# Optimization experiments

Measured on AMD Instinct MI355X. Metric: run time of the kernel, lower is better.

The kernel has to match this reference:

```python
import jax, jax.numpy as jnp
import numpy as np

B, T, D, H, L, F, V = 2, 512, 512, 8, 6, 2048, 32000
EPS = 1e-6


def _ln(x, g, b):
    m = x.mean(-1, keepdims=True)
    v = ((x - m) ** 2).mean(-1, keepdims=True)
    return (x - m) / jnp.sqrt(v + EPS) * g + b


def _mha(qx, kx, qkv_w, qkv_b, ow, ob, mask):
    # Wide heads: each head has dim D (Linear(D, H*D) projections, Linear(H*D, D) output).
    Bq, Tq, _ = qx.shape
    def proj(xx, w, bi):
        return (xx @ w + bi).reshape(Bq, Tq, H, D).transpose(0, 2, 1, 3)  # (B,H,T,D)
    q = proj(qx, qkv_w[0], qkv_b[0])
    k = proj(kx, qkv_w[1], qkv_b[1])
    v = proj(kx, qkv_w[2], qkv_b[2])
    s = jnp.einsum('bhqd,bhkd->bhqk', q, k) / jnp.sqrt(jnp.float32(D))
    if mask is not None:
        s = jnp.where(mask, s, -jnp.inf)
    w = jax.nn.softmax(s, axis=-1)
    o = jnp.einsum('bhqk,bhkd->bhqd', w, v).transpose(0, 2, 1, 3).reshape(Bq, Tq, H * D)
    return o @ ow + ob


def _pe(t, d):
    pos = jnp.arange(t, dtype=jnp.float32)[:, None]
    wl = jnp.exp(jnp.arange(0, d, 2, dtype=jnp.float32) / d * -jnp.log(10000.0))
    pe = jnp.zeros((t, d), dtype=jnp.float32)
    pe = pe.at[:, 0::2].set(jnp.sin(pos * wl))
    pe = pe.at[:, 1::2].set(jnp.cos(pos * wl))
    return pe


def _forward(x, y, enc_emb, dec_emb, enc_qkv_w, enc_qkv_b, enc_out_w, enc_out_b,
             enc_ln1_g, enc_ln1_b, enc_ff_w1, enc_ff_b1, enc_ff_w2, enc_ff_b2,
             enc_ln2_g, enc_ln2_b, dec_sa_qkv_w, dec_sa_qkv_b, dec_sa_out_w, dec_sa_out_b,
             dec_ln1_g, dec_ln1_b, dec_ca_qkv_w, dec_ca_qkv_b, dec_ca_out_w, dec_ca_out_b,
             dec_ln2_g, dec_ln2_b, dec_ff_w1, dec_ff_b1, dec_ff_w2, dec_ff_b2,
             dec_ln3_g, dec_ln3_b, head_w, head_b):
    pe = _pe(T, D)
    scale = jnp.sqrt(jnp.float32(D))
    # ---- encoder ----
    h = enc_emb[x] * scale + pe  # (B,T,D)
    for i in range(L):
        a = _mha(h, h, enc_qkv_w[i], enc_qkv_b[i], enc_out_w[i], enc_out_b[i], None)
        h = _ln(a + h, enc_ln1_g[i], enc_ln1_b[i])
        f = jax.nn.relu(h @ enc_ff_w1[i] + enc_ff_b1[i]) @ enc_ff_w2[i] + enc_ff_b2[i]
        h = _ln(f + h, enc_ln2_g[i], enc_ln2_b[i])
    # ---- decoder ----
    causal = jnp.tril(jnp.ones((T, T), dtype=bool))[None, None]  # (1,1,T,T)
    d = dec_emb[y] * scale + pe
    for i in range(L):
        a = _mha(d, d, dec_sa_qkv_w[i], dec_sa_qkv_b[i], dec_sa_out_w[i], dec_sa_out_b[i], causal)
        d = _ln(a + d, dec_ln1_g[i], dec_ln1_b[i])
        c = _mha(d, h, dec_ca_qkv_w[i], dec_ca_qkv_b[i], dec_ca_out_w[i], dec_ca_out_b[i], None)
        d = _ln(c + d, dec_ln2_g[i], dec_ln2_b[i])
        f = jax.nn.relu(d @ dec_ff_w1[i] + dec_ff_b1[i]) @ dec_ff_w2[i] + dec_ff_b2[i]
        d = _ln(f + d, dec_ln3_g[i], dec_ln3_b[i])
    return d @ head_w + head_b  # (B,T,V) logits


def setup_inputs() -> dict:
    key = jax.random.key(0)
    ks = iter(jax.random.split(key, 40))
    def nrm(shape):
        return jax.random.normal(next(ks), shape, dtype=jnp.float32) * 0.02
    HD = H * D
    return {
        'x': jax.random.randint(next(ks), (B, T), 0, V, dtype=jnp.int32),
        'y': jax.random.randint(next(ks), (B, T), 0, V, dtype=jnp.int32),
        'enc_emb': nrm((V, D)), 'dec_emb': nrm((V, D)),
        'enc_qkv_w': nrm((L, 3, D, HD)), 'enc_qkv_b': jnp.zeros((L, 3, HD)),
        'enc_out_w': nrm((L, HD, D)), 'enc_out_b': jnp.zeros((L, D)),
        'enc_ln1_g': jnp.ones((L, D)), 'enc_ln1_b': jnp.zeros((L, D)),
        'enc_ff_w1': nrm((L, D, F)), 'enc_ff_b1': jnp.zeros((L, F)),
        'enc_ff_w2': nrm((L, F, D)), 'enc_ff_b2': jnp.zeros((L, D)),
        'enc_ln2_g': jnp.ones((L, D)), 'enc_ln2_b': jnp.zeros((L, D)),
        'dec_sa_qkv_w': nrm((L, 3, D, HD)), 'dec_sa_qkv_b': jnp.zeros((L, 3, HD)),
        'dec_sa_out_w': nrm((L, HD, D)), 'dec_sa_out_b': jnp.zeros((L, D)),
        'dec_ln1_g': jnp.ones((L, D)), 'dec_ln1_b': jnp.zeros((L, D)),
        'dec_ca_qkv_w': nrm((L, 3, D, HD)), 'dec_ca_qkv_b': jnp.zeros((L, 3, HD)),
        'dec_ca_out_w': nrm((L, HD, D)), 'dec_ca_out_b': jnp.zeros((L, D)),
        'dec_ln2_g': jnp.ones((L, D)), 'dec_ln2_b': jnp.zeros((L, D)),
        'dec_ff_w1': nrm((L, D, F)), 'dec_ff_b1': jnp.zeros((L, F)),
        'dec_ff_w2': nrm((L, F, D)), 'dec_ff_b2': jnp.zeros((L, D)),
        'dec_ln3_g': jnp.ones((L, D)), 'dec_ln3_b': jnp.zeros((L, D)),
        'head_w': nrm((D, V)), 'head_b': jnp.zeros((V,)),
    }


def reference(x, y, enc_emb, dec_emb, enc_qkv_w, enc_qkv_b, enc_out_w, enc_out_b,
              enc_ln1_g, enc_ln1_b, enc_ff_w1, enc_ff_b1, enc_ff_w2, enc_ff_b2,
              enc_ln2_g, enc_ln2_b, dec_sa_qkv_w, dec_sa_qkv_b, dec_sa_out_w, dec_sa_out_b,
              dec_ln1_g, dec_ln1_b, dec_ca_qkv_w, dec_ca_qkv_b, dec_ca_out_w, dec_ca_out_b,
              dec_ln2_g, dec_ln2_b, dec_ff_w1, dec_ff_b1, dec_ff_w2, dec_ff_b2,
              dec_ln3_g, dec_ln3_b, head_w, head_b):
    return _forward(x, y, enc_emb, dec_emb, enc_qkv_w, enc_qkv_b, enc_out_w, enc_out_b,
                    enc_ln1_g, enc_ln1_b, enc_ff_w1, enc_ff_b1, enc_ff_w2, enc_ff_b2,
                    enc_ln2_g, enc_ln2_b, dec_sa_qkv_w, dec_sa_qkv_b, dec_sa_out_w, dec_sa_out_b,
                    dec_ln1_g, dec_ln1_b, dec_ca_qkv_w, dec_ca_qkv_b, dec_ca_out_w, dec_ca_out_b,
                    dec_ln2_g, dec_ln2_b, dec_ff_w1, dec_ff_b1, dec_ff_w2, dec_ff_b2,
                    dec_ln3_g, dec_ln3_b, head_w, head_b)
```

## Files before the change

kernel.cpp:

```cpp
#include <hip/hip_runtime.h>
#include <hip/hip_bf16.h>

#define B_ 2
#define T_ 512
#define D_ 512
#define H_ 8
#define L_ 6
#define F_ 2048
#define V_ 32000
#define BT_ (B_ * T_)
#define HD_ (H_ * D_)
#define BH_ (B_ * H_)

typedef __attribute__((ext_vector_type(8))) short short8;
typedef __attribute__((ext_vector_type(4))) short short4v;
typedef __attribute__((ext_vector_type(4))) float f32x4;

__device__ __forceinline__ short f2b(float f) {
  __hip_bfloat16 h = __float2bfloat16(f);
  short u; __builtin_memcpy(&u, &h, 2); return u;
}
__device__ __forceinline__ void store_c(float* p, float v) { *p = v; }
__device__ __forceinline__ void store_c(short* p, float v) { *p = f2b(v); }

__global__ __launch_bounds__(256) void embed_kernel(
    const int* __restrict__ tok, const float* __restrict__ emb,
    float* __restrict__ out, short* __restrict__ out16)
{
  const int row = blockIdx.x;
  const int t = row & (T_ - 1);
  const int token = tok[row];
  const float* e = emb + (size_t)token * D_;
  float* o = out + (size_t)row * D_;
  short* o16 = out16 + (size_t)row * D_;
  const float scale = sqrtf((float)D_);
  const float nl = -logf(10000.0f);
  for (int d = threadIdx.x; d < D_; d += 256) {
    int i = d >> 1;
    float wl = expf(nl * (2.0f * (float)i) / (float)D_);
    float ang = (float)t * wl;
    float pe = (d & 1) ? cosf(ang) : sinf(ang);
    float v = e[d] * scale + pe;
    o[d] = v; o16[d] = f2b(v);
  }
}

template<bool BTM, typename OutT, int BM>
__global__ __launch_bounds__(256, 3) void mfma_gemm(
    const short* __restrict__ A, long lda, long a_hi, long a_lo,
    const void* __restrict__ Bv, long ldb, long b_hi, long b_lo,
    OutT* __restrict__ C, long ldc, long c_hi, long c_lo, long pstride,
    short* __restrict__ Ct, int trans_hh,
    int K, int nh, int ksplit, float scale,
    const float* __restrict__ bias, long bias_stride)
{
  constexpr int SA = BM + 1;
  constexpr int AU = BM / 32;
  constexpr int WRN = (BM == 128) ? 2 : 1;
  constexpr int WN  = 128 / (4 / WRN);
  constexpr int NR  = WN / 16;
  __shared__ short8 As8[8 * SA];
  __shared__ short8 Bs8[8 * 129];
  const int tid = threadIdx.x;
  const int bh = blockIdx.z / ksplit;
  const int kz = blockIdx.z - bh * ksplit;
  const int bb = bh / nh, hh = bh - bb * nh;
  const short* Ab = A + (long)bb * a_hi + (long)hh * a_lo;
  const short* Bbs = (const short*)Bv + (long)bb * b_hi + (long)hh * b_lo;
  const float* Bbf = (const float*)Bv + (long)bb * b_hi + (long)hh * b_lo;
  OutT* Cb = C + (long)bb * c_hi + (long)hh * c_lo + (long)kz * pstride;

  const int gx = gridDim.x, gy = gridDim.y;
  const int nwg = gx * gy;
  int lin = blockIdx.y * gx + blockIdx.x;
  {
    const int xcd = lin & 7, idx = lin >> 3;
    const int q = nwg >> 3, r = nwg & 7;
    lin = (xcd < r ? xcd * (q + 1) : r * (q + 1) + (xcd - r) * q) + idx;
  }
  const int bn = (lin / gy) * 128;
  const int bm = (lin % gy) * BM;

  const int klen = K / ksplit, kbase = kz * klen;
  const int lane = tid & 63, wid = tid >> 6;
  const int wr = (WRN == 2) ? (wid >> 1) : 0;
  const int wc = (WRN == 2) ? (wid & 1) : wid;
  const int lg = lane >> 4, r16 = lane & 15;

  int arow[AU], acol[AU];
#pragma unroll
  for (int u = 0; u < AU; ++u) { int o = u * 256 + tid; arow[u] = o >> 3; acol[u] = o & 7; }
  const int ncol = tid & 127, nsh = tid >> 7;

  short8 pa[AU];
  short8 pbt[4];
  float  pbn[4][8];

  auto load = [&](int k0) {
#pragma unroll
    for (int u = 0; u < AU; ++u)
      pa[u] = *(const short8*)(Ab + (long)(bm + arow[u]) * lda + (k0 + acol[u] * 8));
    if constexpr (BTM) {
#pragma unroll
      for (int u = 0; u < 4; ++u)
        pbt[u] = *(const short8*)(Bbs + (long)(bn + (u * 256 + tid) / 8) * ldb + (k0 + ((u * 256 + tid) & 7) * 8));
    } else {
      const float* s = Bbf + (long)(k0 + nsh * 32) * ldb + (bn + ncol);
#pragma unroll
      for (int i = 0; i < 4; ++i)
#pragma unroll
        for (int j = 0; j < 8; ++j)
          pbn[i][j] = s[(long)(i * 8 + j) * ldb];
    }
  };
  auto stage = [&]() {
#pragma unroll
    for (int u = 0; u < AU; ++u) As8[acol[u] * SA + arow[u]] = pa[u];
    if constexpr (BTM) {
#pragma unroll
      for (int u = 0; u < 4; ++u)
        Bs8[((u * 256 + tid) & 7) * 129 + (u * 256 + tid) / 8] = pbt[u];
    } else {
#pragma unroll
      for (int i = 0; i < 4; ++i) {
        short8 v;
#pragma unroll
        for (int j = 0; j < 8; ++j) v[j] = f2b(pbn[i][j]);
        Bs8[(nsh * 4 + i) * 129 + ncol] = v;
      }
    }
  };

  f32x4 acc[4][NR] = {};
  auto domfma = [&]() {
#pragma unroll
    for (int kb = 0; kb < 2; ++kb) {
      const int cha = (kb * 4 + lg) * SA;
      const int chb = (kb * 4 + lg) * 129;
      short8 a0 = As8[cha + wr * 64 +  0 + r16];
      short8 a1 = As8[cha + wr * 64 + 16 + r16];
      short8 a2 = As8[cha + wr * 64 + 32 + r16];
      short8 a3 = As8[cha + wr * 64 + 48 + r16];
#pragma unroll
      for (int n = 0; n < NR; ++n) {
        short8 bfr = Bs8[chb + wc * WN + n * 16 + r16];
        acc[0][n] = __builtin_amdgcn_mfma_f32_16x16x32_bf16(a0, bfr, acc[0][n], 0, 0, 0);
        acc[1][n] = __builtin_amdgcn_mfma_f32_16x16x32_bf16(a1, bfr, acc[1][n], 0, 0, 0);
        acc[2][n] = __builtin_amdgcn_mfma_f32_16x16x32_bf16(a2, bfr, acc[2][n], 0, 0, 0);
        acc[3][n] = __builtin_amdgcn_mfma_f32_16x16x32_bf16(a3, bfr, acc[3][n], 0, 0, 0);
      }
    }
  };

  load(kbase);
  stage();
  __syncthreads();
  const int nsteps = klen >> 6;
  for (int t = 0; t < nsteps; ++t) {
    const bool more = (t + 1 < nsteps);
    if (more) load(kbase + (t + 1) * 64);
    domfma();
    if (more) { __syncthreads(); stage(); __syncthreads(); }
  }

  const float* bp = bias ? bias + (long)hh * bias_stride : nullptr;
  if (hh == trans_hh) {
#pragma unroll
    for (int m = 0; m < 4; ++m)
#pragma unroll
      for (int n = 0; n < NR; ++n) {
        const int col = bn + wc * WN + n * 16 + r16;
        const float badd = bp ? bp[col] : 0.0f;
        short4v sv;
#pragma unroll
        for (int rr = 0; rr < 4; ++rr) sv[rr] = f2b(acc[m][n][rr] * scale + badd);
        *(short4v*)(Ct + (long)col * BT_ + (bm + wr * 64 + m * 16 + lg * 4)) = sv;
      }
  } else {
#pragma unroll
    for (int m = 0; m < 4; ++m)
#pragma unroll
      for (int rr = 0; rr < 4; ++rr) {
        const int row = bm + wr * 64 + m * 16 + lg * 4 + rr;
        OutT* crow = Cb + (long)row * ldc + bn + wc * WN + r16;
#pragma unroll
        for (int n = 0; n < NR; ++n) {
          float v = acc[m][n][rr] * scale;
          if (bp) v += bp[bn + wc * WN + n * 16 + r16];
          store_c(&crow[n * 16], v);
        }
      }
  }
}

__global__ __launch_bounds__(256) void reduce_bias_relu_bf16(
    const float* __restrict__ P, long pstride, int ks,
    const float* __restrict__ bias, short* __restrict__ out, long mn, int N)
{
  const long i = ((long)blockIdx.x * 256 + threadIdx.x) * 4;
  if (i >= mn) return;
  float4 s = *(const float4*)(P + i);
  for (int z = 1; z < ks; ++z) {
    float4 t = *(const float4*)(P + (long)z * pstride + i);
    s.x += t.x; s.y += t.y; s.z += t.z; s.w += t.w;
  }
  const int col = (int)(i % N);
  s.x += bias[col]; s.y += bias[col + 1]; s.z += bias[col + 2]; s.w += bias[col + 3];
  short4v o;
  o[0] = f2b(fmaxf(s.x, 0.f)); o[1] = f2b(fmaxf(s.y, 0.f));
  o[2] = f2b(fmaxf(s.z, 0.f)); o[3] = f2b(fmaxf(s.w, 0.f));
  *(short4v*)(out + i) = o;
}

__global__ __launch_bounds__(256) void reduce_ln_kernel(
    const float* __restrict__ P, long pstride, int ks,
    const float* __restrict__ bias, float* __restrict__ hbuf, short* __restrict__ h16,
    const float* __restrict__ gam, const float* __restrict__ bet)
{
  __shared__ float red[256];
  const int row = blockIdx.x, tid = threadIdx.x;
  const long base = (long)row * D_;
  float s0 = hbuf[base + tid] + bias[tid];
  float s1 = hbuf[base + tid + 256] + bias[tid + 256];
  for (int z = 0; z < ks; ++z) {
    s0 += P[(long)z * pstride + base + tid];
    s1 += P[(long)z * pstride + base + tid + 256];
  }
  red[tid] = s0 + s1; __syncthreads();
  for (int o = 128; o > 0; o >>= 1) { if (tid < o) red[tid] += red[tid + o]; __syncthreads(); }
  const float mean = red[0] * (1.0f / D_); __syncthreads();
  const float d0 = s0 - mean, d1 = s1 - mean;
  red[tid] = d0 * d0 + d1 * d1; __syncthreads();
  for (int o = 128; o > 0; o >>= 1) { if (tid < o) red[tid] += red[tid + o]; __syncthreads(); }
  const float inv = rsqrtf(red[0] * (1.0f / D_) + 1e-6f);
  const float v0 = d0 * inv * gam[tid] + bet[tid];
  const float v1 = d1 * inv * gam[tid + 256] + bet[tid + 256];
  hbuf[base + tid] = v0;       h16[base + tid] = f2b(v0);
  hbuf[base + tid + 256] = v1; h16[base + tid + 256] = f2b(v1);
}

__global__ __launch_bounds__(256) void softmax_kernel(
    const float* __restrict__ S, short* __restrict__ P, int causal)
{
  __shared__ float red[256];
  const int q = blockIdx.x, bh = blockIdx.y, tid = threadIdx.x;
  const float* row = S + ((size_t)bh * T_ + q) * T_;
  short* prow = P + ((size_t)bh * T_ + q) * T_;
  const int n = causal ? (q + 1) : T_;
  const float v0 = row[tid], v1 = row[tid + 256];
  const bool in0 = tid < n, in1 = (tid + 256) < n;
  red[tid] = fmaxf(in0 ? v0 : -3.0e38f, in1 ? v1 : -3.0e38f);
  __syncthreads();
  for (int o = 128; o > 0; o >>= 1) { if (tid < o) red[tid] = fmaxf(red[tid], red[tid + o]); __syncthreads(); }
  const float m = red[0]; __syncthreads();
  const float e0 = in0 ? expf(v0 - m) : 0.0f;
  const float e1 = in1 ? expf(v1 - m) : 0.0f;
  red[tid] = e0 + e1; __syncthreads();
  for (int o = 128; o > 0; o >>= 1) { if (tid < o) red[tid] += red[tid + o]; __syncthreads(); }
  const float inv = 1.0f / red[0];
  prow[tid] = f2b(e0 * inv);
  prow[tid + 256] = f2b(e1 * inv);
}

extern "C" void kernel_launch(void* const* d_in, const int* in_sizes, int n_in,
                              void* d_out, int out_size, void* d_ws, size_t ws_size,
                              hipStream_t stream)
{
  const int*   x         = (const int*)d_in[0];
  const int*   y         = (const int*)d_in[1];
  const float* enc_emb   = (const float*)d_in[2];
  const float* dec_emb   = (const float*)d_in[3];
  const float* enc_qkv_w = (const float*)d_in[4];
  const float* enc_qkv_b = (const float*)d_in[5];
  const float* enc_out_w = (const float*)d_in[6];
  const float* enc_out_b = (const float*)d_in[7];
  const float* enc_ln1_g = (const float*)d_in[8];
  const float* enc_ln1_b = (const float*)d_in[9];
  const float* enc_ff_w1 = (const float*)d_in[10];
  const float* enc_ff_b1 = (const float*)d_in[11];
  const float* enc_ff_w2 = (const float*)d_in[12];
  const float* enc_ff_b2 = (const float*)d_in[13];
  const float* enc_ln2_g = (const float*)d_in[14];
  const float* enc_ln2_b = (const float*)d_in[15];
  const float* dec_sa_qkv_w = (const float*)d_in[16];
  const float* dec_sa_qkv_b = (const float*)d_in[17];
  const float* dec_sa_out_w = (const float*)d_in[18];
  const float* dec_sa_out_b = (const float*)d_in[19];
  const float* dec_ln1_g = (const float*)d_in[20];
  const float* dec_ln1_b = (const float*)d_in[21];
  const float* dec_ca_qkv_w = (const float*)d_in[22];
  const float* dec_ca_qkv_b = (const float*)d_in[23];
  const float* dec_ca_out_w = (const float*)d_in[24];
  const float* dec_ca_out_b = (const float*)d_in[25];
  const float* dec_ln2_g = (const float*)d_in[26];
  const float* dec_ln2_b = (const float*)d_in[27];
  const float* dec_ff_w1 = (const float*)d_in[28];
  const float* dec_ff_b1 = (const float*)d_in[29];
  const float* dec_ff_w2 = (const float*)d_in[30];
  const float* dec_ff_b2 = (const float*)d_in[31];
  const float* dec_ln3_g = (const float*)d_in[32];
  const float* dec_ln3_b = (const float*)d_in[33];
  const float* head_w    = (const float*)d_in[34];
  const float* head_b    = (const float*)d_in[35];
  float* out = (float*)d_out;

  char* wsb = (char*)d_ws;
  size_t off = 0;
  auto carve = [&](size_t bytes) { char* p = wsb + off; off += (bytes + 255) & ~255ull; return p; };
  float* h    = (float*)carve((size_t)BT_ * D_ * 4);
  float* dd   = (float*)carve((size_t)BT_ * D_ * 4);
  short* hb16 = (short*)carve((size_t)BT_ * D_ * 2);
  short* db16 = (short*)carve((size_t)BT_ * D_ * 2);
  short* Qb   = (short*)carve((size_t)BT_ * HD_ * 2);
  short* Kb   = (short*)carve((size_t)BT_ * HD_ * 2);
  short* Vt   = (short*)carve((size_t)HD_ * BT_ * 2);
  float* Sb   = (float*)carve((size_t)BH_ * T_ * T_ * 4);
  short* Pb   = (short*)carve((size_t)BH_ * T_ * T_ * 2);
  short* Ob   = Qb;
  short* mid  = Qb;
  (void)ws_size;

  dim3 blk(256);
  const long TT  = (long)T_ * T_;
  const long THD = (long)T_ * HD_;
  const long WQKV = (long)D_ * HD_;

  auto gemm = [&](bool bt, bool of32, bool bm64,
                  const short* A, long lda, long a_hi, long a_lo,
                  const void* Bp, long ldb, long b_hi, long b_lo,
                  void* Cp, long ldc, long c_hi, long c_lo, long pstride,
                  short* Ct, int trans_hh,
                  int M, int N, int K, int batch, int nh, int ksplit,
                  float scale, const float* bias, long bstride) {
    dim3 grd(N / 128, M / (bm64 ? 64 : 128), batch * ksplit);
    if (bm64) {
      if (bt) {
        if (of32) mfma_gemm<true , float, 64><<<grd, blk, 0, stream>>>(A, lda, a_hi, a_lo, Bp, ldb, b_hi, b_lo,
            (float*)Cp, ldc, c_hi, c_lo, pstride, Ct, trans_hh, K, nh, ksplit, scale, bias, bstride);
        else      mfma_gemm<true , short, 64><<<grd, blk, 0, stream>>>(A, lda, a_hi, a_lo, Bp, ldb, b_hi, b_lo,
            (short*)Cp, ldc, c_hi, c_lo, pstride, Ct, trans_hh, K, nh, ksplit, scale, bias, bstride);
      } else {
        if (of32) mfma_gemm<false, float, 64><<<grd, blk, 0, stream>>>(A, lda, a_hi, a_lo, Bp, ldb, b_hi, b_lo,
            (float*)Cp, ldc, c_hi, c_lo, pstride, Ct, trans_hh, K, nh, ksplit, scale, bias, bstride);
        else      mfma_gemm<false, short, 64><<<grd, blk, 0, stream>>>(A, lda, a_hi, a_lo, Bp, ldb, b_hi, b_lo,
            (short*)Cp, ldc, c_hi, c_lo, pstride, Ct, trans_hh, K, nh, ksplit, scale, bias, bstride);
      }
    } else {
      if (of32) mfma_gemm<false, float, 128><<<grd, blk, 0, stream>>>(A, lda, a_hi, a_lo, Bp, ldb, b_hi, b_lo,
          (float*)Cp, ldc, c_hi, c_lo, pstride, Ct, trans_hh, K, nh, ksplit, scale, bias, bstride);
      else      mfma_gemm<false, short, 128><<<grd, blk, 0, stream>>>(A, lda, a_hi, a_lo, Bp, ldb, b_hi, b_lo,
          (short*)Cp, ldc, c_hi, c_lo, pstride, Ct, trans_hh, K, nh, ksplit, scale, bias, bstride);
    }
  };

  auto attention = [&](const short* qsrc, const short* kvsrc, bool self,
                       const float* qkvw, const float* qkvb,
                       const float* ow, const float* ob,
                       float* resid, short* resid16, int causal,
                       const float* lng, const float* lnb) {
    if (self) {
      gemm(false, false, true, qsrc, D_, 0, 0, qkvw, HD_, 0, WQKV,
           Qb, HD_, 0, (long)(Kb - Qb), 0, Vt, 2,
           BT_, HD_, D_, 3, 3, 1, 1.0f, qkvb, HD_);
    } else {
      gemm(false, false, true, qsrc, D_, 0, 0, qkvw, HD_, 0, 0,
           Qb, HD_, 0, 0, 0, nullptr, -1,
           BT_, HD_, D_, 1, 1, 1, 1.0f, qkvb, 0);
      gemm(false, false, true, kvsrc, D_, 0, 0, qkvw + WQKV, HD_, 0, WQKV,
           Kb, HD_, 0, 0, 0, Vt, 1,
           BT_, HD_, D_, 2, 2, 1, 1.0f, qkvb + HD_, HD_);
    }
    gemm(true, true, true, Qb, HD_, THD, D_, Kb, HD_, THD, D_,
         Sb, T_, (long)H_ * TT, TT, 0, nullptr, -1,
         T_, T_, D_, BH_, H_, 1, 0.044194173824159216f, nullptr, 0);
    softmax_kernel<<<dim3(T_, BH_), blk, 0, stream>>>(Sb, Pb, causal);
    gemm(true, false, true, Pb, T_, (long)H_ * TT, TT, Vt, BT_, T_, (long)D_ * BT_,
         Ob, HD_, THD, D_, 0, nullptr, -1,
         T_, D_, T_, BH_, H_, 1, 1.0f, nullptr, 0);
    gemm(false, true, true, Ob, HD_, 0, 0, ow, D_, 0, 0,
         Sb, D_, 0, 0, (long)BT_ * D_, nullptr, -1,
         BT_, D_, HD_, 1, 1, 8, 1.0f, nullptr, 0);
    reduce_ln_kernel<<<dim3(BT_), blk, 0, stream>>>(
        Sb, (long)BT_ * D_, 8, ob, resid, resid16, lng, lnb);
  };

  auto ffn = [&](float* resid, short* resid16,
                 const float* w1, const float* b1,
                 const float* w2, const float* b2,
                 const float* lng, const float* lnb) {
    gemm(false, true, true, resid16, D_, 0, 0, w1, F_, 0, 0,
         Sb, F_, 0, 0, (long)BT_ * F_, nullptr, -1,
         BT_, F_, D_, 1, 1, 2, 1.0f, nullptr, 0);
    reduce_bias_relu_bf16<<<dim3(BT_ * F_ / 1024), blk, 0, stream>>>(
        Sb, (long)BT_ * F_, 2, b1, mid, (long)BT_ * F_, F_);
    gemm(false, true, true, mid, F_, 0, 0, w2, D_, 0, 0,
         Sb, D_, 0, 0, (long)BT_ * D_, nullptr, -1,
         BT_, D_, F_, 1, 1, 8, 1.0f, nullptr, 0);
    reduce_ln_kernel<<<dim3(BT_), blk, 0, stream>>>(
        Sb, (long)BT_ * D_, 8, b2, resid, resid16, lng, lnb);
  };

  embed_kernel<<<dim3(BT_), blk, 0, stream>>>(x, enc_emb, h, hb16);
  for (int i = 0; i < L_; ++i) {
    attention(hb16, hb16, true,
              enc_qkv_w + (size_t)i * 3 * WQKV, enc_qkv_b + (size_t)i * 3 * HD_,
              enc_out_w + (size_t)i * HD_ * D_, enc_out_b + (size_t)i * D_,
              h, hb16, 0, enc_ln1_g + (size_t)i * D_, enc_ln1_b + (size_t)i * D_);
    ffn(h, hb16, enc_ff_w1 + (size_t)i * D_ * F_, enc_ff_b1 + (size_t)i * F_,
        enc_ff_w2 + (size_t)i * F_ * D_, enc_ff_b2 + (size_t)i * D_,
        enc_ln2_g + (size_t)i * D_, enc_ln2_b + (size_t)i * D_);
  }

  embed_kernel<<<dim3(BT_), blk, 0, stream>>>(y, dec_emb, dd, db16);
  for (int i = 0; i < L_; ++i) {
    attention(db16, db16, true,
              dec_sa_qkv_w + (size_t)i * 3 * WQKV, dec_sa_qkv_b + (size_t)i * 3 * HD_,
              dec_sa_out_w + (size_t)i * HD_ * D_, dec_sa_out_b + (size_t)i * D_,
              dd, db16, 1, dec_ln1_g + (size_t)i * D_, dec_ln1_b + (size_t)i * D_);
    attention(db16, hb16, false,
              dec_ca_qkv_w + (size_t)i * 3 * WQKV, dec_ca_qkv_b + (size_t)i * 3 * HD_,
              dec_ca_out_w + (size_t)i * HD_ * D_, dec_ca_out_b + (size_t)i * D_,
              dd, db16, 0, dec_ln2_g + (size_t)i * D_, dec_ln2_b + (size_t)i * D_);
    ffn(dd, db16, dec_ff_w1 + (size_t)i * D_ * F_, dec_ff_b1 + (size_t)i * F_,
        dec_ff_w2 + (size_t)i * F_ * D_, dec_ff_b2 + (size_t)i * D_,
        dec_ln3_g + (size_t)i * D_, dec_ln3_b + (size_t)i * D_);
  }

  gemm(false, true, false, db16, D_, 0, 0, head_w, V_, 0, 0,
       out, V_, 0, 0, 0, nullptr, -1,
       BT_, V_, D_, 1, 1, 1, 1.0f, head_b, 0);
}
```

Baseline: 2.392 ms.

## Fuse softmax into PV GEMM, skip causal tiles, fuse FFN bias+ReLU, reduce split-K

```diff
diff --git a/kernel.cpp b/kernel.cpp
--- a/kernel.cpp
+++ b/kernel.cpp
@@ -50,14 +50,14 @@
     const short* __restrict__ A, long lda, long a_hi, long a_lo,
     const void* __restrict__ Bv, long ldb, long b_hi, long b_lo,
     OutT* __restrict__ C, long ldc, long c_hi, long c_lo, long pstride,
-    short* __restrict__ Ct, int trans_hh,
+    short* __restrict__ Ct, int trans_hh, int relu, int causal_skip,
     int K, int nh, int ksplit, float scale,
     const float* __restrict__ bias, long bias_stride)
 {
   constexpr int SA = BM + 1;
   constexpr int AU = BM / 32;
   constexpr int WRN = (BM == 128) ? 2 : 1;
-  constexpr int WN  = 128 / (4 / WRN);
+  constexpr int WN  = (BM == 128) ? 64 : 32;
   constexpr int NR  = WN / 16;
   __shared__ short8 As8[8 * SA];
   __shared__ short8 Bs8[8 * 129];
@@ -80,6 +80,7 @@
   }
   const int bn = (lin / gy) * 128;
   const int bm = (lin % gy) * BM;
+  if (causal_skip && bn > bm + BM - 1) return;
 
   const int klen = K / ksplit, kbase = kz * klen;
   const int lane = tid & 63, wid = tid >> 6;
@@ -90,6 +91,9 @@
   int arow[AU], acol[AU];
 #pragma unroll
   for (int u = 0; u < AU; ++u) { int o = u * 256 + tid; arow[u] = o >> 3; acol[u] = o & 7; }
+  int brow[4], bcol[4];
+#pragma unroll
+  for (int u = 0; u < 4; ++u) { int o = u * 256 + tid; brow[u] = o >> 3; bcol[u] = o & 7; }
   const int ncol = tid & 127, nsh = tid >> 7;
 
   short8 pa[AU];
@@ -103,7 +107,7 @@
     if constexpr (BTM) {
 #pragma unroll
       for (int u = 0; u < 4; ++u)
-        pbt[u] = *(const short8*)(Bbs + (long)(bn + (u * 256 + tid) / 8) * ldb + (k0 + ((u * 256 + tid) & 7) * 8));
+        pbt[u] = *(const short8*)(Bbs + (long)(bn + brow[u]) * ldb + (k0 + bcol[u] * 8));
     } else {
       const float* s = Bbf + (long)(k0 + nsh * 32) * ldb + (bn + ncol);
 #pragma unroll
@@ -118,8 +122,7 @@
     for (int u = 0; u < AU; ++u) As8[acol[u] * SA + arow[u]] = pa[u];
     if constexpr (BTM) {
 #pragma unroll
-      for (int u = 0; u < 4; ++u)
-        Bs8[((u * 256 + tid) & 7) * 129 + (u * 256 + tid) / 8] = pbt[u];
+      for (int u = 0; u < 4; ++u) Bs8[bcol[u] * 129 + brow[u]] = pbt[u];
     } else {
 #pragma unroll
       for (int i = 0; i < 4; ++i) {
@@ -187,29 +190,155 @@
         for (int n = 0; n < NR; ++n) {
           float v = acc[m][n][rr] * scale;
           if (bp) v += bp[bn + wc * WN + n * 16 + r16];
+          if (relu) v = fmaxf(v, 0.0f);
           store_c(&crow[n * 16], v);
         }
       }
   }
 }
 
-__global__ __launch_bounds__(256) void reduce_bias_relu_bf16(
-    const float* __restrict__ P, long pstride, int ks,
-    const float* __restrict__ bias, short* __restrict__ out, long mn, int N)
+__global__ __launch_bounds__(256, 3) void smpv_kernel(
+    const float* __restrict__ S, const short* __restrict__ Vt,
+    short* __restrict__ O, int causal)
 {
-  const long i = ((long)blockIdx.x * 256 + threadIdx.x) * 4;
-  if (i >= mn) return;
-  float4 s = *(const float4*)(P + i);
-  for (int z = 1; z < ks; ++z) {
-    float4 t = *(const float4*)(P + (long)z * pstride + i);
-    s.x += t.x; s.y += t.y; s.z += t.z; s.w += t.w;
-  }
-  const int col = (int)(i % N);
-  s.x += bias[col]; s.y += bias[col + 1]; s.z += bias[col + 2]; s.w += bias[col + 3];
-  short4v o;
-  o[0] = f2b(fmaxf(s.x, 0.f)); o[1] = f2b(fmaxf(s.y, 0.f));
-  o[2] = f2b(fmaxf(s.z, 0.f)); o[3] = f2b(fmaxf(s.w, 0.f));
-  *(short4v*)(out + i) = o;
+  __shared__ short8 As8[8 * 65];
+  __shared__ short8 Bs8[8 * 129];
+  __shared__ float mrow[64], linv[64];
+
+  const int tid = threadIdx.x;
+  const int bh = blockIdx.z;
+  const int b = bh >> 3, hh = bh & 7;
+  const int bm = blockIdx.y * 64;
+  const int bn = blockIdx.x * 128;
+  const int lane = tid & 63, w4 = tid >> 6;
+  const int lg = lane >> 4, r16 = lane & 15;
+
+  const float* Sb = S + (long)bh * T_ * T_;
+  const short* Vb = Vt + ((long)hh * D_ + bn) * BT_ + (long)b * T_;
+
+  {
+    const int row = tid >> 2, sub = tid & 3;
+    const int qrow = bm + row;
+    const int ncols = causal ? (qrow + 1) : T_;
+    const float* sp = Sb + (long)qrow * T_;
+    float mx = -3.0e38f;
+    for (int i = 0; i < 32; ++i) {
+      const int c0 = (sub + i * 4) * 4;
+      if (c0 < ncols) {
+        float4 v = *(const float4*)(sp + c0);
+        mx = fmaxf(mx, v.x);
+        if (c0 + 1 < ncols) mx = fmaxf(mx, v.y);
+        if (c0 + 2 < ncols) mx = fmaxf(mx, v.z);
+        if (c0 + 3 < ncols) mx = fmaxf(mx, v.w);
+      }
+    }
+    mx = fmaxf(mx, __shfl_xor(mx, 1));
+    mx = fmaxf(mx, __shfl_xor(mx, 2));
+    float sm = 0.0f;
+    for (int i = 0; i < 32; ++i) {
+      const int c0 = (sub + i * 4) * 4;
+      if (c0 < ncols) {
+        float4 v = *(const float4*)(sp + c0);
+        sm += expf(v.x - mx);
+        if (c0 + 1 < ncols) sm += expf(v.y - mx);
+        if (c0 + 2 < ncols) sm += expf(v.z - mx);
+        if (c0 + 3 < ncols) sm += expf(v.w - mx);
+      }
+    }
+    sm += __shfl_xor(sm, 1);
+    sm += __shfl_xor(sm, 2);
+    if (sub == 0) { mrow[row] = mx; linv[row] = 1.0f / sm; }
+  }
+  __syncthreads();
+
+  int arow[2], acol[2];
+#pragma unroll
+  for (int u = 0; u < 2; ++u) { int o = u * 256 + tid; arow[u] = o >> 3; acol[u] = o & 7; }
+  int brow[4], bcol[4];
+#pragma unroll
+  for (int u = 0; u < 4; ++u) { int o = u * 256 + tid; brow[u] = o >> 3; bcol[u] = o & 7; }
+
+  float4 pa[2][2];
+  short8 pbt[4];
+
+  auto load = [&](int k0) {
+#pragma unroll
+    for (int u = 0; u < 2; ++u) {
+      const float* s = Sb + (long)(bm + arow[u]) * T_ + (k0 + acol[u] * 8);
+      pa[u][0] = *(const float4*)(s);
+      pa[u][1] = *(const float4*)(s + 4);
+    }
+#pragma unroll
+    for (int u = 0; u < 4; ++u)
+      pbt[u] = *(const short8*)(Vb + (long)brow[u] * BT_ + (k0 + bcol[u] * 8));
+  };
+  auto stage = [&](int k0, bool mask) {
+#pragma unroll
+    for (int u = 0; u < 2; ++u) {
+      const int row = arow[u];
+      const int qrow = bm + row;
+      const float m = mrow[row];
+      const float vals[8] = {pa[u][0].x, pa[u][0].y, pa[u][0].z, pa[u][0].w,
+                             pa[u][1].x, pa[u][1].y, pa[u][1].z, pa[u][1].w};
+      short8 v;
+#pragma unroll
+      for (int j = 0; j < 8; ++j) {
+        const bool valid = !mask || (k0 + acol[u] * 8 + j <= qrow);
+        v[j] = f2b(valid ? expf(vals[j] - m) : 0.0f);
+      }
+      As8[acol[u] * 65 + row] = v;
+    }
+#pragma unroll
+    for (int u = 0; u < 4; ++u) Bs8[bcol[u] * 129 + brow[u]] = pbt[u];
+  };
+
+  f32x4 acc[4][2] = {};
+  auto domfma = [&]() {
+#pragma unroll
+    for (int kb = 0; kb < 2; ++kb) {
+      const int cha = (kb * 4 + lg) * 65;
+      const int chb = (kb * 4 + lg) * 129;
+      short8 a0 = As8[cha +  0 + r16];
+      short8 a1 = As8[cha + 16 + r16];
+      short8 a2 = As8[cha + 32 + r16];
+      short8 a3 = As8[cha + 48 + r16];
+#pragma unroll
+      for (int n = 0; n < 2; ++n) {
+        short8 bfr = Bs8[chb + w4 * 32 + n * 16 + r16];
+        acc[0][n] = __builtin_amdgcn_mfma_f32_16x16x32_bf16(a0, bfr, acc[0][n], 0, 0, 0);
+        acc[1][n] = __builtin_amdgcn_mfma_f32_16x16x32_bf16(a1, bfr, acc[1][n], 0, 0, 0);
+        acc[2][n] = __builtin_amdgcn_mfma_f32_16x16x32_bf16(a2, bfr, acc[2][n], 0, 0, 0);
+        acc[3][n] = __builtin_amdgcn_mfma_f32_16x16x32_bf16(a3, bfr, acc[3][n], 0, 0, 0);
+      }
+    }
+  };
+
+  const int nsteps = causal ? ((bm >> 6) + 1) : (T_ >> 6);
+  load(0);
+  stage(0, causal && (0 >= bm));
+  __syncthreads();
+  for (int t = 0; t < nsteps; ++t) {
+    const bool more = (t + 1 < nsteps);
+    if (more) load((t + 1) * 64);
+    domfma();
+    if (more) {
+      __syncthreads();
+      stage((t + 1) * 64, causal && ((t + 1) * 64 >= bm));
+      __syncthreads();
+    }
+  }
+
+  short* Ob = O + ((long)b * T_ + bm) * HD_ + hh * D_ + bn;
+#pragma unroll
+  for (int m = 0; m < 4; ++m)
+#pragma unroll
+    for (int rr = 0; rr < 4; ++rr) {
+      const int row = m * 16 + lg * 4 + rr;
+      const float il = linv[row];
+#pragma unroll
+      for (int n = 0; n < 2; ++n)
+        Ob[(long)row * HD_ + w4 * 32 + n * 16 + r16] = f2b(acc[m][n][rr] * il);
+    }
 }
 
 __global__ __launch_bounds__(256) void reduce_ln_kernel(
@@ -237,29 +366,6 @@
   const float v1 = d1 * inv * gam[tid + 256] + bet[tid + 256];
   hbuf[base + tid] = v0;       h16[base + tid] = f2b(v0);
   hbuf[base + tid + 256] = v1; h16[base + tid + 256] = f2b(v1);
-}
-
-__global__ __launch_bounds__(256) void softmax_kernel(
-    const float* __restrict__ S, short* __restrict__ P, int causal)
-{
-  __shared__ float red[256];
-  const int q = blockIdx.x, bh = blockIdx.y, tid = threadIdx.x;
-  const float* row = S + ((size_t)bh * T_ + q) * T_;
-  short* prow = P + ((size_t)bh * T_ + q) * T_;
-  const int n = causal ? (q + 1) : T_;
-  const float v0 = row[tid], v1 = row[tid + 256];
-  const bool in0 = tid < n, in1 = (tid + 256) < n;
-  red[tid] = fmaxf(in0 ? v0 : -3.0e38f, in1 ? v1 : -3.0e38f);
-  __syncthreads();
-  for (int o = 128; o > 0; o >>= 1) { if (tid < o) red[tid] = fmaxf(red[tid], red[tid + o]); __syncthreads(); }
-  const float m = red[0]; __syncthreads();
-  const float e0 = in0 ? expf(v0 - m) : 0.0f;
-  const float e1 = in1 ? expf(v1 - m) : 0.0f;
-  red[tid] = e0 + e1; __syncthreads();
-  for (int o = 128; o > 0; o >>= 1) { if (tid < o) red[tid] += red[tid + o]; __syncthreads(); }
-  const float inv = 1.0f / red[0];
-  prow[tid] = f2b(e0 * inv);
-  prow[tid + 256] = f2b(e1 * inv);
 }
 
 extern "C" void kernel_launch(void* const* d_in, const int* in_sizes, int n_in,
@@ -315,7 +421,6 @@
   short* Kb   = (short*)carve((size_t)BT_ * HD_ * 2);
   short* Vt   = (short*)carve((size_t)HD_ * BT_ * 2);
   float* Sb   = (float*)carve((size_t)BH_ * T_ * T_ * 4);
-  short* Pb   = (short*)carve((size_t)BH_ * T_ * T_ * 2);
   short* Ob   = Qb;
   short* mid  = Qb;
   (void)ws_size;
@@ -325,7 +430,7 @@
   const long THD = (long)T_ * HD_;
   const long WQKV = (long)D_ * HD_;
 
-  auto gemm = [&](bool bt, bool of32, bool bm64,
+  auto gemm = [&](bool bt, bool of32, bool bm64, int relu, int cskip,
                   const short* A, long lda, long a_hi, long a_lo,
                   const void* Bp, long ldb, long b_hi, long b_lo,
                   void* Cp, long ldc, long c_hi, long c_lo, long pstride,
@@ -336,20 +441,20 @@
     if (bm64) {
       if (bt) {
         if (of32) mfma_gemm<true , float, 64><<<grd, blk, 0, stream>>>(A, lda, a_hi, a_lo, Bp, ldb, b_hi, b_lo,
-            (float*)Cp, ldc, c_hi, c_lo, pstride, Ct, trans_hh, K, nh, ksplit, scale, bias, bstride);
+            (float*)Cp, ldc, c_hi, c_lo, pstride, Ct, trans_hh, relu, cskip, K, nh, ksplit, scale, bias, bstride);
         else      mfma_gemm<true , short, 64><<<grd, blk, 0, stream>>>(A, lda, a_hi, a_lo, Bp, ldb, b_hi, b_lo,
-            (short*)Cp, ldc, c_hi, c_lo, pstride, Ct, trans_hh, K, nh, ksplit, scale, bias, bstride);
+            (short*)Cp, ldc, c_hi, c_lo, pstride, Ct, trans_hh, relu, cskip, K, nh, ksplit, scale, bias, bstride);
       } else {
         if (of32) mfma_gemm<false, float, 64><<<grd, blk, 0, stream>>>(A, lda, a_hi, a_lo, Bp, ldb, b_hi, b_lo,
-            (float*)Cp, ldc, c_hi, c_lo, pstride, Ct, trans_hh, K, nh, ksplit, scale, bias, bstride);
+            (float*)Cp, ldc, c_hi, c_lo, pstride, Ct, trans_hh, relu, cskip, K, nh, ksplit, scale, bias, bstride);
         else      mfma_gemm<false, short, 64><<<grd, blk, 0, stream>>>(A, lda, a_hi, a_lo, Bp, ldb, b_hi, b_lo,
-            (short*)Cp, ldc, c_hi, c_lo, pstride, Ct, trans_hh, K, nh, ksplit, scale, bias, bstride);
+            (short*)Cp, ldc, c_hi, c_lo, pstride, Ct, trans_hh, relu, cskip, K, nh, ksplit, scale, bias, bstride);
       }
     } else {
       if (of32) mfma_gemm<false, float, 128><<<grd, blk, 0, stream>>>(A, lda, a_hi, a_lo, Bp, ldb, b_hi, b_lo,
-          (float*)Cp, ldc, c_hi, c_lo, pstride, Ct, trans_hh, K, nh, ksplit, scale, bias, bstride);
+          (float*)Cp, ldc, c_hi, c_lo, pstride, Ct, trans_hh, relu, cskip, K, nh, ksplit, scale, bias, bstride);
       else      mfma_gemm<false, short, 128><<<grd, blk, 0, stream>>>(A, lda, a_hi, a_lo, Bp, ldb, b_hi, b_lo,
-          (short*)Cp, ldc, c_hi, c_lo, pstride, Ct, trans_hh, K, nh, ksplit, scale, bias, bstride);
+          (short*)Cp, ldc, c_hi, c_lo, pstride, Ct, trans_hh, relu, cskip, K, nh, ksplit, scale, bias, bstride);
     }
   };
 
@@ -359,45 +464,40 @@
                        float* resid, short* resid16, int causal,
                        const float* lng, const float* lnb) {
     if (self) {
-      gemm(false, false, true, qsrc, D_, 0, 0, qkvw, HD_, 0, WQKV,
+      gemm(false, false, true, 0, 0, qsrc, D_, 0, 0, qkvw, HD_, 0, WQKV,
            Qb, HD_, 0, (long)(Kb - Qb), 0, Vt, 2,
            BT_, HD_, D_, 3, 3, 1, 1.0f, qkvb, HD_);
     } else {
-      gemm(false, false, true, qsrc, D_, 0, 0, qkvw, HD_, 0, 0,
+      gemm(false, false, true, 0, 0, qsrc, D_, 0, 0, qkvw, HD_, 0, 0,
            Qb, HD_, 0, 0, 0, nullptr, -1,
            BT_, HD_, D_, 1, 1, 1, 1.0f, qkvb, 0);
-      gemm(false, false, true, kvsrc, D_, 0, 0, qkvw + WQKV, HD_, 0, WQKV,
+      gemm(false, false, true, 0, 0, kvsrc, D_, 0, 0, qkvw + WQKV, HD_, 0, WQKV,
            Kb, HD_, 0, 0, 0, Vt, 1,
            BT_, HD_, D_, 2, 2, 1, 1.0f, qkvb + HD_, HD_);
     }
-    gemm(true, true, true, Qb, HD_, THD, D_, Kb, HD_, THD, D_,
+    gemm(true, true, true, 0, causal, Qb, HD_, THD, D_, Kb, HD_, THD, D_,
          Sb, T_, (long)H_ * TT, TT, 0, nullptr, -1,
          T_, T_, D_, BH_, H_, 1, 0.044194173824159216f, nullptr, 0);
-    softmax_kernel<<<dim3(T_, BH_), blk, 0, stream>>>(Sb, Pb, causal);
-    gemm(true, false, true, Pb, T_, (long)H_ * TT, TT, Vt, BT_, T_, (long)D_ * BT_,
-         Ob, HD_, THD, D_, 0, nullptr, -1,
-         T_, D_, T_, BH_, H_, 1, 1.0f, nullptr, 0);
-    gemm(false, true, true, Ob, HD_, 0, 0, ow, D_, 0, 0,
+    smpv_kernel<<<dim3(D_ / 128, T_ / 64, BH_), blk, 0, stream>>>(Sb, Vt, Ob, causal);
+    gemm(false, true, true, 0, 0, Ob, HD_, 0, 0, ow, D_, 0, 0,
          Sb, D_, 0, 0, (long)BT_ * D_, nullptr, -1,
-         BT_, D_, HD_, 1, 1, 8, 1.0f, nullptr, 0);
+         BT_, D_, HD_, 1, 1, 4, 1.0f, nullptr, 0);
     reduce_ln_kernel<<<dim3(BT_), blk, 0, stream>>>(
-        Sb, (long)BT_ * D_, 8, ob, resid, resid16, lng, lnb);
+        Sb, (long)BT_ * D_, 4, ob, resid, resid16, lng, lnb);
   };
 
   auto ffn = [&](float* resid, short* resid16,
                  const float* w1, const float* b1,
                  const float* w2, const float* b2,
                  const float* lng, const float* lnb) {
-    gemm(false, true, true, resid16, D_, 0, 0, w1, F_, 0, 0,
-         Sb, F_, 0, 0, (long)BT_ * F_, nullptr, -1,
-         BT_, F_, D_, 1, 1, 2, 1.0f, nullptr, 0);
-    reduce_bias_relu_bf16<<<dim3(BT_ * F_ / 1024), blk, 0, stream>>>(
-        Sb, (long)BT_ * F_, 2, b1, mid, (long)BT_ * F_, F_);
-    gemm(false, true, true, mid, F_, 0, 0, w2, D_, 0, 0,
+    gemm(false, false, true, 1, 0, resid16, D_, 0, 0, w1, F_, 0, 0,
+         mid, F_, 0, 0, 0, nullptr, -1,
+         BT_, F_, D_, 1, 1, 1, 1.0f, b1, 0);
+    gemm(false, true, true, 0, 0, mid, F_, 0, 0, w2, D_, 0, 0,
          Sb, D_, 0, 0, (long)BT_ * D_, nullptr, -1,
-         BT_, D_, F_, 1, 1, 8, 1.0f, nullptr, 0);
+         BT_, D_, F_, 1, 1, 4, 1.0f, nullptr, 0);
     reduce_ln_kernel<<<dim3(BT_), blk, 0, stream>>>(
-        Sb, (long)BT_ * D_, 8, b2, resid, resid16, lng, lnb);
+        Sb, (long)BT_ * D_, 4, b2, resid, resid16, lng, lnb);
   };
 
   embed_kernel<<<dim3(BT_), blk, 0, stream>>>(x, enc_emb, h, hb16);
@@ -426,7 +526,7 @@
         dec_ln3_g + (size_t)i * D_, dec_ln3_b + (size_t)i * D_);
   }
 
-  gemm(false, true, false, db16, D_, 0, 0, head_w, V_, 0, 0,
+  gemm(false, true, false, 0, 0, db16, D_, 0, 0, head_w, V_, 0, 0,
        out, V_, 0, 0, 0, nullptr, -1,
        BT_, V_, D_, 1, 1, 1, 1.0f, head_b, 0);
 }
```

New measurement: 2.853 ms. 19.3% more time.
